# Kernel optimization log

Hardware: AMD Instinct MI355X
Metric: run time of the kernel (lower is better)

## Reference

```python
import jax, jax.numpy as jnp
from jax import lax
import numpy as np

G = 32        # voxel grid resolution per axis (pres=vres=1 -> voxel = floor(coord))
N = 100000    # number of points
C = 96        # hidden_dim == input_dim


def _voxelize(feats, coords):
    """initial_voxelize: average point features per voxel. Returns (grid (G^3,C), occ (G^3,) bool, flat idx)."""
    vox = jnp.clip(jnp.floor(coords).astype(jnp.int32), 0, G - 1)
    flat = (vox[:, 0] * G + vox[:, 1]) * G + vox[:, 2]
    sums = jax.ops.segment_sum(feats, flat, num_segments=G ** 3)
    cnt = jax.ops.segment_sum(jnp.ones((feats.shape[0],), feats.dtype), flat, num_segments=G ** 3)
    grid = sums / jnp.maximum(cnt, 1.0)[:, None]
    return grid, cnt > 0


def _sconv(feats, coords, conv_w, lin_w, lin_b):
    """SConv3d: voxelize -> submanifold 3x3x3 conv (outputs only at occupied voxels)
    -> trilinear devoxelize (missing voxels contribute 0) -> + Linear(feats)."""
    Cin = feats.shape[1]
    Cout = conv_w.shape[0]
    grid, occ = _voxelize(feats, coords)
    g = grid.reshape(G, G, G, Cin).transpose(3, 0, 1, 2)[None]          # (1,Cin,G,G,G)
    out = lax.conv_general_dilated(g, conv_w, (1, 1, 1), 'SAME',
                                   dimension_numbers=('NCDHW', 'OIDHW', 'NCDHW'))
    out = out * occ.reshape(1, 1, G, G, G)                               # submanifold: keep input coords only
    outv = out[0].transpose(1, 2, 3, 0).reshape(G ** 3, Cout)            # (G^3,Cout)
    base = jnp.floor(coords)
    f = coords - base                                                    # trilinear fractions (N,3)
    basei = base.astype(jnp.int32)
    devox = jnp.zeros((feats.shape[0], Cout), feats.dtype)
    for dx in (0, 1):
        for dy in (0, 1):
            for dz in (0, 1):
                c = basei + jnp.array([dx, dy, dz], jnp.int32)
                valid = jnp.all((c >= 0) & (c < G), axis=1)
                cc = jnp.clip(c, 0, G - 1)
                flc = (cc[:, 0] * G + cc[:, 1]) * G + cc[:, 2]
                w = ((f[:, 0] if dx else 1.0 - f[:, 0]) *
                     (f[:, 1] if dy else 1.0 - f[:, 1]) *
                     (f[:, 2] if dz else 1.0 - f[:, 2]))
                w = w * (valid & occ[flc]).astype(w.dtype)
                devox = devox + outv[flc] * w[:, None]
    return devox + feats @ lin_w.T + lin_b


def setup_inputs() -> dict:
    key = jax.random.key(0)
    ks = jax.random.split(key, 20)
    def conv(k, o, i):
        return jax.random.normal(k, (o, i, 3, 3, 3), jnp.float32) / np.sqrt(i * 27)
    def lin(k, o, i):
        k1, k2 = jax.random.split(k)
        return (jax.random.normal(k1, (o, i), jnp.float32) / np.sqrt(i),
                jax.random.normal(k2, (o,), jnp.float32) * 0.01)
    wq_lw, wq_lb = lin(ks[3], C, C)
    wh_lw, wh_lb = lin(ks[4], C, C)
    att_lw, att_lb = lin(ks[5], C, 2 * C)
    v_lw, v_lb = lin(ks[6], 1, C)
    upd_lw, upd_lb = lin(ks[7], C, 2 * C)
    return {
        'hidden': jax.random.normal(ks[0], (N, C), jnp.float32),
        'query': jax.random.normal(ks[1], (N, C), jnp.float32),
        'coords': jax.random.uniform(ks[2], (N, 3), jnp.float32) * G,
        'wq_conv': conv(ks[8], C, C), 'wq_lw': wq_lw, 'wq_lb': wq_lb,
        'wh_conv': conv(ks[9], C, C), 'wh_lw': wh_lw, 'wh_lb': wh_lb,
        'att_conv': conv(ks[10], C, 2 * C), 'att_lw': att_lw, 'att_lb': att_lb,
        'v_conv': conv(ks[11], 1, C), 'v_lw': v_lw, 'v_lb': v_lb,
        'upd_conv': conv(ks[12], C, 2 * C), 'upd_lw': upd_lw, 'upd_lb': upd_lb,
    }


def reference(hidden, query, coords,
              wq_conv, wq_lw, wq_lb,
              wh_conv, wh_lw, wh_lb,
              att_conv, att_lw, att_lb,
              v_conv, v_lw, v_lb,
              upd_conv, upd_lw, upd_lb):
    q = _sconv(query, coords, wq_conv, wq_lw, wq_lb)           # (N,C)
    h = _sconv(hidden, coords, wh_conv, wh_lw, wh_lb)          # (N,C)
    hx = jnp.concatenate([h, q], axis=1)                        # (N,2C)
    energy = jnp.tanh(_sconv(hx, coords, att_conv, att_lw, att_lb))
    attn = _sconv(energy, coords, v_conv, v_lw, v_lb)           # (N,1)
    context = attn * h                                          # attention-gated hidden
    qcat = jnp.concatenate([q, context], axis=1)                # (N,2C)
    return jnp.tanh(_sconv(qcat, coords, upd_conv, upd_lw, upd_lb))
```

## Files before the change

### kernel.cpp

```cpp
#include <hip/hip_runtime.h>
#include <math.h>


#define GD 32
#define NV (GD*GD*GD)
#define CH 96

typedef _Float16 half8 __attribute__((ext_vector_type(8)));
typedef _Float16 half4 __attribute__((ext_vector_type(4)));
typedef float f32x4 __attribute__((ext_vector_type(4)));


__global__ void k_prep(const float* __restrict__ coords, int* __restrict__ flat,
                       unsigned* __restrict__ cnt, int n) {
  int i = blockIdx.x * 256 + threadIdx.x;
  if (i >= n) return;
  float x = coords[3*i], y = coords[3*i+1], z = coords[3*i+2];
  int ix = (int)floorf(x); ix = ix < 0 ? 0 : (ix > 31 ? 31 : ix);
  int iy = (int)floorf(y); iy = iy < 0 ? 0 : (iy > 31 ? 31 : iy);
  int iz = (int)floorf(z); iz = iz < 0 ? 0 : (iz > 31 ? 31 : iz);
  int f = (ix << 10) + (iy << 5) + iz;
  flat[i] = f;
  atomicAdd(&cnt[f], 1u);
}

__global__ __launch_bounds__(1024) void k_scan(
    const unsigned* __restrict__ cnt, unsigned* __restrict__ base,
    unsigned* __restrict__ cur, float* __restrict__ inv) {
  __shared__ unsigned part[1024];
  int tid = threadIdx.x;
  int b0 = tid * 32;
  unsigned s = 0;
  for (int i = 0; i < 32; ++i) s += cnt[b0 + i];
  part[tid] = s;
  __syncthreads();
  for (int off = 1; off < 1024; off <<= 1) {
    unsigned t = (tid >= off) ? part[tid - off] : 0u;
    __syncthreads();
    if (tid >= off) part[tid] += t;
    __syncthreads();
  }
  unsigned run = part[tid] - s;
  for (int i = 0; i < 32; ++i) {
    int v = b0 + i;
    unsigned c = cnt[v];
    base[v] = run; cur[v] = run;
    inv[v] = c ? 1.0f / (float)c : 0.0f;
    run += c;
  }
}

__global__ void k_fill(const int* __restrict__ flat, unsigned* __restrict__ cur,
                       int* __restrict__ order, int n) {
  int p = blockIdx.x * 256 + threadIdx.x;
  if (p >= n) return;
  unsigned pos = atomicAdd(&cur[flat[p]], 1u);
  order[pos] = p;
}

template<int SCALED, int PAIR, int SRCF16>
__global__ void k_voxavg(const void* __restrict__ src, const float* __restrict__ scale,
                         const unsigned* __restrict__ base, const unsigned* __restrict__ cnt,
                         const float* __restrict__ inv, const int* __restrict__ order,
                         void* __restrict__ dst,
                         const void* __restrict__ src2, void* __restrict__ dst2) {
  int e = blockIdx.x * 256 + threadIdx.x;
  const void* sp = src; void* d = dst;
  if (PAIR && e >= NV * 24) { e -= NV * 24; sp = src2; d = dst2; }
  int v = e / 24, c4 = e - v * 24;
  unsigned b = base[v], c = cnt[v];
  f32x4 s = {0.f, 0.f, 0.f, 0.f};
  for (unsigned i = 0; i < c; ++i) {
    int p = order[b + i];
    f32x4 x;
    if (SRCF16) {
      half4 hx = __builtin_nontemporal_load(reinterpret_cast<const half4*>(sp) + p * 24 + c4);
      x = (f32x4){(float)hx[0], (float)hx[1], (float)hx[2], (float)hx[3]};
    } else {
      x = __builtin_nontemporal_load(reinterpret_cast<const f32x4*>(sp) + p * 24 + c4);
    }
    if (SCALED) x *= scale[p];
    s += x;
  }
  s *= inv[v];
  union { _Float16 h; unsigned short u; } h0, h1, h2, h3;
  h0.h = (_Float16)s.x; h1.h = (_Float16)s.y; h2.h = (_Float16)s.z; h3.h = (_Float16)s.w;
  ushort4 o; o.x = h0.u; o.y = h1.u; o.z = h2.u; o.w = h3.u;
  reinterpret_cast<ushort4*>(d)[e] = o;
}


__device__ __forceinline__ void wpack_one(int e, const float* __restrict__ w,
                                          _Float16* __restrict__ wp, int nch) {
  int j = e & 7; int l = (e >> 3) & 63; int r = e >> 9;
  int cot = r % 6; r /= 6; int chk = r % nch; int tap = r / nch;
  int Ci = nch * 32;
  int ci = chk * 32 + (l >> 4) * 8 + j;
  int co = cot * 16 + (l & 15);
  wp[e] = (_Float16)w[(co * Ci + ci) * 27 + tap];
}

__device__ __forceinline__ void linpack_one(int e, const float* __restrict__ w,
                                            _Float16* __restrict__ wl, int kb) {
  int j = e & 7; int l = (e >> 3) & 63; int r = e >> 9;
  int nt = r % 6; int kt = r / 6;
  int Ci = kb * 32;
  int ci = kt * 32 + (l >> 4) * 8 + j;
  int co = nt * 16 + (l & 15);
  wl[e] = (_Float16)w[co * Ci + ci];
}

#define WP3 (27*3*6*512)
#define WP6 (27*6*6*512)
#define WL3 (3*6*512)
#define WL6 (6*6*512)
#define PACK_TOTAL (2*WP3 + 2*WP6 + 2*WL3 + 2*WL6 + 27*96)

__global__ void k_packall(
    const float* __restrict__ wq, const float* __restrict__ wh,
    const float* __restrict__ wa, const float* __restrict__ wu,
    const float* __restrict__ lq, const float* __restrict__ lh,
    const float* __restrict__ la, const float* __restrict__ lu,
    const float* __restrict__ wvc,
    _Float16* __restrict__ wpq, _Float16* __restrict__ wph,
    _Float16* __restrict__ wpa, _Float16* __restrict__ wpu,
    _Float16* __restrict__ wlq, _Float16* __restrict__ wlh,
    _Float16* __restrict__ wla, _Float16* __restrict__ wlu,
    float* __restrict__ wtv) {
  int e = blockIdx.x * 256 + threadIdx.x;
  if (e < WP3) { wpack_one(e, wq, wpq, 3); return; } e -= WP3;
  if (e < WP3) { wpack_one(e, wh, wph, 3); return; } e -= WP3;
  if (e < WP6) { wpack_one(e, wa, wpa, 6); return; } e -= WP6;
  if (e < WP6) { wpack_one(e, wu, wpu, 6); return; } e -= WP6;
  if (e < WL3) { linpack_one(e, lq, wlq, 3); return; } e -= WL3;
  if (e < WL3) { linpack_one(e, lh, wlh, 3); return; } e -= WL3;
  if (e < WL6) { linpack_one(e, la, wla, 6); return; } e -= WL6;
  if (e < WL6) { linpack_one(e, lu, wlu, 6); return; } e -= WL6;
  if (e < 27 * 96) {
    int ci = e % 96, tap = e / 96;
    wtv[e] = wvc[ci * 27 + tap];
  }
}

template<int NCH, int PAIR>
__global__ __launch_bounds__(384, 4) void k_conv_mfma(
    const _Float16* __restrict__ gA, const _Float16* __restrict__ gB,
    const half8* __restrict__ wp, _Float16* __restrict__ out,
    const _Float16* __restrict__ gA2, const half8* __restrict__ wp2,
    _Float16* __restrict__ out2) {
  __shared__ unsigned short ls[12 * 34 * 40];
  int bid = blockIdx.x;
  const _Float16* ga = gA; const _Float16* gb = gB;
  const half8* w = wp; _Float16* o = out;
  if (PAIR && bid >= 512) { bid -= 512; ga = gA2; gb = gA2; w = wp2; o = out2; }
  int bx = bid >> 4, y0 = (bid & 15) * 2;
  int tid = threadIdx.x;
  int lane = tid & 63, wv = tid >> 6;
  int msel = wv & 1, npair = wv >> 1;
  int lrow = lane & 15, quad = lane >> 4;

  f32x4 acc[2][2];
#pragma unroll
  for (int i = 0; i < 2; ++i)
#pragma unroll
    for (int j = 0; j < 2; ++j) acc[i][j] = (f32x4){0.f, 0.f, 0.f, 0.f};

  for (int chunk = 0; chunk < NCH; ++chunk) {
    const _Float16* g = (NCH == 6 && chunk >= 3) ? gb : ga;
    int cbase = ((NCH == 6 && chunk >= 3) ? chunk - 3 : chunk) * 32;
    __syncthreads();
    for (int e = tid; e < 12 * 34 * 4; e += 384) {
      int ciu = e & 3; int zc = e >> 2;
      int zz = zc % 34; int sc = zc / 34;
      int dx = sc >> 2, dyy = sc & 3;
      int x = bx + dx - 1, y = y0 + dyy - 1, zv = zz - 1;
      uint4 val = {0u, 0u, 0u, 0u};
      if ((unsigned)x < 32u && (unsigned)y < 32u && (unsigned)zv < 32u)
        val = *reinterpret_cast<const uint4*>(
            g + (size_t)((x << 10) + (y << 5) + zv) * CH + cbase + ciu * 8);
      *reinterpret_cast<uint4*>(&ls[(sc * 34 + zz) * 40 + ciu * 8]) = val;
    }
    __syncthreads();
#pragma unroll
    for (int dx9 = 0; dx9 < 3; ++dx9)
#pragma unroll
      for (int dy9 = 0; dy9 < 3; ++dy9) {
        int sc = dx9 * 4 + msel + dy9;
        const unsigned short* lbase = &ls[(sc * 34) * 40 + quad * 8];
        int tap0 = (dx9 * 3 + dy9) * 3;
#pragma unroll
        for (int dz = 0; dz < 3; ++dz) {
          half8 a0 = *reinterpret_cast<const half8*>(&lbase[(lrow + dz) * 40]);
          half8 a1 = *reinterpret_cast<const half8*>(&lbase[(16 + lrow + dz) * 40]);
          const half8* wb = w + ((size_t)((tap0 + dz) * NCH + chunk) * 6 + npair * 2) * 64 + lane;
          half8 b0 = wb[0];
          half8 b1 = wb[64];
          acc[0][0] = __builtin_amdgcn_mfma_f32_16x16x32_f16(a0, b0, acc[0][0], 0, 0, 0);
          acc[1][0] = __builtin_amdgcn_mfma_f32_16x16x32_f16(a1, b0, acc[1][0], 0, 0, 0);
          acc[0][1] = __builtin_amdgcn_mfma_f32_16x16x32_f16(a0, b1, acc[0][1], 0, 0, 0);
          acc[1][1] = __builtin_amdgcn_mfma_f32_16x16x32_f16(a1, b1, acc[1][1], 0, 0, 0);
        }
      }
  }
  int y = y0 + msel;
  int vb = (bx << 10) + (y << 5);
#pragma unroll
  for (int mt = 0; mt < 2; ++mt)
#pragma unroll
    for (int nb = 0; nb < 2; ++nb)
#pragma unroll
      for (int r = 0; r < 4; ++r) {
        int z = mt * 16 + quad * 4 + r;
        o[(size_t)(vb + z) * CH + (npair * 2 + nb) * 16 + lrow] = (_Float16)acc[mt][nb][r];
      }
}

__global__ __launch_bounds__(128) void k_conv3d_v(
    const _Float16* __restrict__ g, const float* __restrict__ wt, float* __restrict__ out) {
  __shared__ float lg[9 * 34 * 33];
  __shared__ float red[128];
  int bx = blockIdx.x >> 5, by = blockIdx.x & 31;
  int tid = threadIdx.x;
  int z = tid & 31, part = tid >> 5;
  float acc = 0.f;
  for (int chunk = 0; chunk < 3; ++chunk) {
    int c0 = chunk * 32;
    __syncthreads();
    for (int e = tid; e < 9 * 34 * 32; e += 128) {
      int col = e / 1088; int rem = e - col * 1088;
      int zz = rem >> 5; int c = rem & 31;
      int x = bx + col / 3 - 1;
      int y = by + (col - (col / 3) * 3) - 1;
      int zv = zz - 1;
      float val = 0.f;
      if ((unsigned)x < 32u && (unsigned)y < 32u && (unsigned)zv < 32u)
        val = (float)g[((x << 10) + (y << 5) + zv) * CH + c0 + c];
      lg[(col * 34 + zz) * 33 + c] = val;
    }
    __syncthreads();
    for (int tap = 0; tap < 27; ++tap) {
      int cc = tap / 3, dz = tap - cc * 3;
      const float* lgp = &lg[(cc * 34 + z + dz) * 33 + part * 8];
      const float* wp = wt + tap * CH + c0 + part * 8;
#pragma unroll
      for (int c = 0; c < 8; ++c) acc += lgp[c] * wp[c];
    }
  }
  red[tid] = acc;
  __syncthreads();
  if (part == 0)
    out[(bx << 10) + (by << 5) + z] = red[z] + red[z + 32] + red[z + 64] + red[z + 96];
}


__device__ __forceinline__ void corner_one(
    const float* __restrict__ coords, const unsigned* __restrict__ cnt,
    int p, int k, int& flc, float& w) {
  float cx = coords[3*p], cy = coords[3*p+1], cz = coords[3*p+2];
  float bx = floorf(cx), by = floorf(cy), bz = floorf(cz);
  float fx = cx - bx, fy = cy - by, fz = cz - bz;
  int dx = (k >> 2) & 1, dy = (k >> 1) & 1, dzz = k & 1;
  int ix = (int)bx + dx, iy = (int)by + dy, iz = (int)bz + dzz;
  bool valid = ((unsigned)ix < 32u) && ((unsigned)iy < 32u) && ((unsigned)iz < 32u);
  int xc = min(max(ix, 0), 31), yc = min(max(iy, 0), 31), zc = min(max(iz, 0), 31);
  flc = (xc << 10) + (yc << 5) + zc;
  float wx = dx ? fx : 1.f - fx;
  float wy = dy ? fy : 1.f - fy;
  float wz = dzz ? fz : 1.f - fz;
  w = (valid && cnt[flc] > 0u) ? wx * wy * wz : 0.f;
}

template<int KB, int MODE, int PAIR>
__global__ __launch_bounds__(256) void k_point(
    const _Float16* __restrict__ outv, const void* __restrict__ X1, const void* __restrict__ X2,
    const float* __restrict__ scale, const half8* __restrict__ wl,
    const float* __restrict__ lb, const float* __restrict__ vlw,
    const float* __restrict__ coords, const unsigned* __restrict__ cnt,
    void* __restrict__ dst, float* __restrict__ attn_out, int n,
    const _Float16* __restrict__ outv2, const void* __restrict__ X1b,
    const half8* __restrict__ wl2, const float* __restrict__ lb2,
    void* __restrict__ dst2) {
  __shared__ char us[64 * 100 * 4];
  __shared__ int lflc[512];
  __shared__ float lcw[512];
  constexpr int APITCH = KB * 32 + 8;
  constexpr int XF16 = (KB == 6);
  constexpr int OUTF16 = (MODE != 2);
  int tid = threadIdx.x;
  int bid = blockIdx.x;
  const _Float16* ov = outv; const void* x1 = X1;
  const half8* w = wl; const float* b = lb; void* d = dst;
  if (PAIR) {
    int npt = (n + 63) >> 6;
    if (bid >= npt) { bid -= npt; ov = outv2; x1 = X1b; w = wl2; b = lb2; d = dst2; }
  }
  int p0 = bid * 64;

  for (int e = tid; e < 512; e += 256) {
    int j = e >> 3, k = e & 7, p = p0 + j;
    int f = 0; float wgt = 0.f;
    if (p < n) corner_one(coords, cnt, p, k, f, wgt);
    lflc[e] = f; lcw[e] = wgt;
  }

  unsigned short* lsa = reinterpret_cast<unsigned short*>(us);
  constexpr int T4 = 64 * KB * 8;
  for (int e = tid; e < T4; e += 256) {
    int j = e / (KB * 8);
    int q4 = e - j * (KB * 8);
    int p = p0 + j;
    if (XF16) {
      half4 hx = {(_Float16)0.f, (_Float16)0.f, (_Float16)0.f, (_Float16)0.f};
      if (p < n) {
        if (q4 < 24) {
          hx = __builtin_nontemporal_load(reinterpret_cast<const half4*>(x1) + p * 24 + q4);
        } else {
          hx = __builtin_nontemporal_load(reinterpret_cast<const half4*>(X2) + p * 24 + (q4 - 24));
          if (MODE == 2) {
            float sc = scale[p];
            hx = (half4){(_Float16)((float)hx[0] * sc), (_Float16)((float)hx[1] * sc),
                         (_Float16)((float)hx[2] * sc), (_Float16)((float)hx[3] * sc)};
          }
        }
      }
      *reinterpret_cast<half4*>(&lsa[j * APITCH + q4 * 4]) = hx;
    } else {
      f32x4 v = {0.f, 0.f, 0.f, 0.f};
      if (p < n)
        v = __builtin_nontemporal_load(reinterpret_cast<const f32x4*>(x1) + p * 24 + q4);
      union { _Float16 h; unsigned short u; } h0, h1, h2, h3;
      h0.h = (_Float16)v.x; h1.h = (_Float16)v.y; h2.h = (_Float16)v.z; h3.h = (_Float16)v.w;
      ushort4 o; o.x = h0.u; o.y = h1.u; o.z = h2.u; o.w = h3.u;
      *reinterpret_cast<ushort4*>(&lsa[j * APITCH + q4 * 4]) = o;
    }
  }
  __syncthreads();

  int lane = tid & 63, wv = tid >> 6;
  int lrow = lane & 15, quad = lane >> 4;
  f32x4 acc[6];
#pragma unroll
  for (int i = 0; i < 6; ++i) acc[i] = (f32x4){0.f, 0.f, 0.f, 0.f};
#pragma unroll
  for (int kt = 0; kt < KB; ++kt) {
    half8 a = *reinterpret_cast<const half8*>(&lsa[(wv * 16 + lrow) * APITCH + kt * 32 + quad * 8]);
    const half8* wb = w + (size_t)(kt * 6) * 64 + lane;
#pragma unroll
    for (int nt = 0; nt < 6; ++nt)
      acc[nt] = __builtin_amdgcn_mfma_f32_16x16x32_f16(a, wb[(size_t)nt * 64], acc[nt], 0, 0, 0);
  }
  __syncthreads();
  float* lacc = reinterpret_cast<float*>(us);
#pragma unroll
  for (int nt = 0; nt < 6; ++nt)
#pragma unroll
    for (int r = 0; r < 4; ++r)
      lacc[(wv * 16 + quad * 4 + r) * 100 + nt * 16 + lrow] = acc[nt][r];
  __syncthreads();

  int pt = tid >> 2, sub = tid & 3;
  int p = p0 + pt;
  f32x4 a[6];
  const float* lrow_p = &lacc[pt * 100 + sub * 24];
#pragma unroll
  for (int i = 0; i < 6; ++i) a[i] = *reinterpret_cast<const f32x4*>(lrow_p + i * 4);
  const f32x4* lb4 = reinterpret_cast<const f32x4*>(b + sub * 24);
#pragma unroll
  for (int i = 0; i < 6; ++i) a[i] += lb4[i];
#pragma unroll
  for (int k = 0; k < 8; ++k) {
    float wgt = lcw[pt * 8 + k];
    if (wgt != 0.f) {
      const half8* op = reinterpret_cast<const half8*>(ov + (size_t)lflc[pt * 8 + k] * CH + sub * 24);
      half8 o0 = op[0], o1 = op[1], o2 = op[2];
      f32x4 t;
      t = (f32x4){(float)o0[0], (float)o0[1], (float)o0[2], (float)o0[3]}; a[0] += wgt * t;
      t = (f32x4){(float)o0[4], (float)o0[5], (float)o0[6], (float)o0[7]}; a[1] += wgt * t;
      t = (f32x4){(float)o1[0], (float)o1[1], (float)o1[2], (float)o1[3]}; a[2] += wgt * t;
      t = (f32x4){(float)o1[4], (float)o1[5], (float)o1[6], (float)o1[7]}; a[3] += wgt * t;
      t = (f32x4){(float)o2[0], (float)o2[1], (float)o2[2], (float)o2[3]}; a[4] += wgt * t;
      t = (f32x4){(float)o2[4], (float)o2[5], (float)o2[6], (float)o2[7]}; a[5] += wgt * t;
    }
  }
  if (MODE >= 1) {
#pragma unroll
    for (int i = 0; i < 6; ++i) {
      a[i].x = tanhf(a[i].x); a[i].y = tanhf(a[i].y);
      a[i].z = tanhf(a[i].z); a[i].w = tanhf(a[i].w);
    }
  }
  if (p < n) {
    if (OUTF16) {
      _Float16* dh = reinterpret_cast<_Float16*>(d) + (size_t)p * CH + sub * 24;
      uint4* du = reinterpret_cast<uint4*>(dh);
#pragma unroll
      for (int i = 0; i < 3; ++i) {
        union { _Float16 h[8]; uint4 q; } t;
        t.h[0] = (_Float16)a[2*i].x;   t.h[1] = (_Float16)a[2*i].y;
        t.h[2] = (_Float16)a[2*i].z;   t.h[3] = (_Float16)a[2*i].w;
        t.h[4] = (_Float16)a[2*i+1].x; t.h[5] = (_Float16)a[2*i+1].y;
        t.h[6] = (_Float16)a[2*i+1].z; t.h[7] = (_Float16)a[2*i+1].w;
        du[i] = t.q;
      }
    } else {
      f32x4* d4 = reinterpret_cast<f32x4*>(d) + (size_t)p * 24 + sub * 6;
#pragma unroll
      for (int i = 0; i < 6; ++i) d4[i] = a[i];
    }
  }
  if (MODE == 1) {
    const f32x4* vw4 = reinterpret_cast<const f32x4*>(vlw + sub * 24);
    float partial = 0.f;
#pragma unroll
    for (int i = 0; i < 6; ++i) {
      f32x4 vw = vw4[i];
      partial += a[i].x * vw.x + a[i].y * vw.y + a[i].z * vw.z + a[i].w * vw.w;
    }
    partial += __shfl_xor(partial, 1);
    partial += __shfl_xor(partial, 2);
    if (sub == 0 && p < n) attn_out[p] = partial;
  }
}

__global__ void k_attn_final(const float* __restrict__ outvV, const float* __restrict__ vlb,
                             const float* __restrict__ coords, const unsigned* __restrict__ cnt,
                             float* __restrict__ attn, int n) {
  int p = blockIdx.x * 256 + threadIdx.x;
  if (p >= n) return;
  float a = attn[p] + vlb[0];
#pragma unroll
  for (int k = 0; k < 8; ++k) {
    int f; float w;
    corner_one(coords, cnt, p, k, f, w);
    a += w * outvV[f];
  }
  attn[p] = a;
}


extern "C" void kernel_launch(void* const* d_in, const int* in_sizes, int n_in,
                              void* d_out, int out_size, void* d_ws, size_t ws_size,
                              hipStream_t stream) {
  const float* hidden   = (const float*)d_in[0];
  const float* query    = (const float*)d_in[1];
  const float* coords   = (const float*)d_in[2];
  const float* wq_conv  = (const float*)d_in[3];
  const float* wq_lw    = (const float*)d_in[4];
  const float* wq_lb    = (const float*)d_in[5];
  const float* wh_conv  = (const float*)d_in[6];
  const float* wh_lw    = (const float*)d_in[7];
  const float* wh_lb    = (const float*)d_in[8];
  const float* att_conv = (const float*)d_in[9];
  const float* att_lw   = (const float*)d_in[10];
  const float* att_lb   = (const float*)d_in[11];
  const float* v_conv   = (const float*)d_in[12];
  const float* v_lw     = (const float*)d_in[13];
  const float* v_lb     = (const float*)d_in[14];
  const float* upd_conv = (const float*)d_in[15];
  const float* upd_lw   = (const float*)d_in[16];
  const float* upd_lb   = (const float*)d_in[17];
  float* out = (float*)d_out;
  const int n = in_sizes[0] / CH;

  char* wsp = (char*)d_ws;
  auto alloc = [&](size_t bytes) {
    char* r = wsp;
    wsp += (bytes + 255) & ~(size_t)255;
    return r;
  };
  int*      flat  = (int*)     alloc((size_t)n * 4);
  int*      order = (int*)     alloc((size_t)n * 4);
  unsigned* cnt   = (unsigned*)alloc((size_t)NV * 4);
  unsigned* base  = (unsigned*)alloc((size_t)NV * 4);
  unsigned* cur   = (unsigned*)alloc((size_t)NV * 4);
  float*    inv   = (float*)   alloc((size_t)NV * 4);
  float*    attn  = (float*)   alloc((size_t)n * 4);
  float*    wtv   = (float*)   alloc((size_t)27 * 96 * 4);
  _Float16* wpq = (_Float16*)alloc((size_t)WP3 * 2);
  _Float16* wph = (_Float16*)alloc((size_t)WP3 * 2);
  _Float16* wpa = (_Float16*)alloc((size_t)WP6 * 2);
  _Float16* wpu = (_Float16*)alloc((size_t)WP6 * 2);
  _Float16* wlq = (_Float16*)alloc((size_t)WL3 * 2);
  _Float16* wlh = (_Float16*)alloc((size_t)WL3 * 2);
  _Float16* wla = (_Float16*)alloc((size_t)WL6 * 2);
  _Float16* wlu = (_Float16*)alloc((size_t)WL6 * 2);
  _Float16* Hq  = (_Float16*)alloc((size_t)NV * CH * 2);
  _Float16* Hh  = (_Float16*)alloc((size_t)NV * CH * 2);
  _Float16* H1  = (_Float16*)alloc((size_t)NV * CH * 2);
  _Float16* H2  = (_Float16*)alloc((size_t)NV * CH * 2);
  _Float16* O1  = (_Float16*)alloc((size_t)NV * CH * 2);
  _Float16* O2  = (_Float16*)alloc((size_t)NV * CH * 2);
  float* Ov   = (float*)alloc((size_t)NV * 4);
  _Float16* qv   = (_Float16*)alloc((size_t)n * CH * 2);
  _Float16* hv   = (_Float16*)alloc((size_t)n * CH * 2);
  _Float16* ebuf = (_Float16*)alloc((size_t)n * CH * 2);

  const int nb  = (n + 255) / 256;
  const int npt = (n + 63) / 64;
  const int nva = NV * 24 / 256;

  hipMemsetAsync(cnt, 0, (size_t)NV * 4, stream);
  k_prep<<<nb, 256, 0, stream>>>(coords, flat, cnt, n);
  k_scan<<<1, 1024, 0, stream>>>(cnt, base, cur, inv);
  k_fill<<<nb, 256, 0, stream>>>(flat, cur, order, n);
  k_packall<<<(PACK_TOTAL + 255) / 256, 256, 0, stream>>>(
      wq_conv, wh_conv, att_conv, upd_conv, wq_lw, wh_lw, att_lw, upd_lw, v_conv,
      wpq, wph, wpa, wpu, wlq, wlh, wla, wlu, wtv);

  k_voxavg<0,1,0><<<2*nva, 256, 0, stream>>>(query, nullptr, base, cnt, inv, order,
                                             Hq, hidden, Hh);
  k_conv_mfma<3,1><<<1024, 384, 0, stream>>>(Hq, Hq, (const half8*)wpq, O1,
                                             Hh, (const half8*)wph, O2);
  k_point<3,0,1><<<2*npt, 256, 0, stream>>>(O1, query, nullptr, nullptr, (const half8*)wlq,
                                            wq_lb, nullptr, coords, cnt, qv, nullptr, n,
                                            O2, hidden, (const half8*)wlh, wh_lb, hv);

  k_voxavg<0,1,1><<<2*nva, 256, 0, stream>>>(hv, nullptr, base, cnt, inv, order,
                                             H1, qv, H2);
  k_conv_mfma<6,0><<<512, 384, 0, stream>>>(H1, H2, (const half8*)wpa, O1,
                                            nullptr, nullptr, nullptr);
  k_point<6,1,0><<<npt, 256, 0, stream>>>(O1, hv, qv, nullptr, (const half8*)wla,
                                          att_lb, v_lw, coords, cnt, ebuf, attn, n,
                                          nullptr, nullptr, nullptr, nullptr, nullptr);

  k_voxavg<0,0,1><<<nva, 256, 0, stream>>>(ebuf, nullptr, base, cnt, inv, order,
                                           Hq, nullptr, nullptr);
  k_conv3d_v<<<1024, 128, 0, stream>>>(Hq, wtv, Ov);
  k_attn_final<<<nb, 256, 0, stream>>>(Ov, v_lb, coords, cnt, attn, n);

  k_voxavg<1,0,1><<<nva, 256, 0, stream>>>(hv, attn, base, cnt, inv, order,
                                           H1, nullptr, nullptr);
  k_conv_mfma<6,0><<<512, 384, 0, stream>>>(H2, H1, (const half8*)wpu, O1,
                                            nullptr, nullptr, nullptr);
  k_point<6,2,0><<<npt, 256, 0, stream>>>(O1, qv, hv, attn, (const half8*)wlu,
                                          upd_lb, nullptr, coords, cnt, out, nullptr, n,
                                          nullptr, nullptr, nullptr, nullptr, nullptr);
}
```

Before: 691.0 us.

## Move single-output-channel 3D conv onto MFMA with dz taps as GEMM columns

Rewrites the Cin=96 to Cout=1 attention conv as an fp16 MFMA kernel. Each block covers two y rows, stages a swizzled fp16 halo tile in LDS with 16-byte loads, and packs the three dz taps into the N dimension of a 16x16x32 MFMA (13 of 16 columns are zero). A shuffle through LDS then adds the dz-shifted partial sums. This replaces the scalar fp32 FMA loop and its LDS reduction, but wastes most of each MFMA and accumulates with fp16 weights.

Result: faster. 639.1 us (-7.5%).

```diff
diff --git a/kernel.cpp b/kernel.cpp
--- a/kernel.cpp
+++ b/kernel.cpp
@@ -114,7 +114,8 @@
 #define WP6 (27*6*6*512)
 #define WL3 (3*6*512)
 #define WL6 (6*6*512)
-#define PACK_TOTAL (2*WP3 + 2*WP6 + 2*WL3 + 2*WL6 + 27*96)
+#define WV2 (27*512)
+#define PACK_TOTAL (2*WP3 + 2*WP6 + 2*WL3 + 2*WL6 + WV2)
 
 __global__ void k_packall(
     const float* __restrict__ wq, const float* __restrict__ wh,
@@ -126,7 +127,7 @@
     _Float16* __restrict__ wpa, _Float16* __restrict__ wpu,
     _Float16* __restrict__ wlq, _Float16* __restrict__ wlh,
     _Float16* __restrict__ wla, _Float16* __restrict__ wlu,
-    float* __restrict__ wtv) {
+    _Float16* __restrict__ wt2) {
   int e = blockIdx.x * 256 + threadIdx.x;
   if (e < WP3) { wpack_one(e, wq, wpq, 3); return; } e -= WP3;
   if (e < WP3) { wpack_one(e, wh, wph, 3); return; } e -= WP3;
@@ -136,9 +137,12 @@
   if (e < WL3) { linpack_one(e, lh, wlh, 3); return; } e -= WL3;
   if (e < WL6) { linpack_one(e, la, wla, 6); return; } e -= WL6;
   if (e < WL6) { linpack_one(e, lu, wlu, 6); return; } e -= WL6;
-  if (e < 27 * 96) {
-    int ci = e % 96, tap = e / 96;
-    wtv[e] = wvc[ci * 27 + tap];
+  if (e < WV2) {
+    int j = e & 7; int l = (e >> 3) & 63; int r = e >> 9;
+    int col9 = r % 9, chunk = r / 9;
+    int n = l & 15, kq = l >> 4;
+    int ci = chunk * 32 + kq * 8 + j;
+    wt2[e] = (n < 3) ? (_Float16)wvc[ci * 27 + col9 * 3 + n] : (_Float16)0.f;
   }
 }
 
@@ -215,41 +219,69 @@
       }
 }
 
-__global__ __launch_bounds__(128) void k_conv3d_v(
-    const _Float16* __restrict__ g, const float* __restrict__ wt, float* __restrict__ out) {
-  __shared__ float lg[9 * 34 * 33];
-  __shared__ float red[128];
-  int bx = blockIdx.x >> 5, by = blockIdx.x & 31;
+__global__ __launch_bounds__(128) void k_conv3d_v2(
+    const _Float16* __restrict__ g, const _Float16* __restrict__ wt2,
+    float* __restrict__ out) {
+  __shared__ unsigned short ls[12 * 48 * 32];
+  __shared__ float dl[2][48][4];
+  int bid = blockIdx.x;
+  int bx = bid >> 4, y0 = (bid & 15) * 2;
   int tid = threadIdx.x;
-  int z = tid & 31, part = tid >> 5;
-  float acc = 0.f;
+  int lane = tid & 63, wv = tid >> 6;
+  int lrow = lane & 15, quad = lane >> 4;
+
+  f32x4 acc[3];
+#pragma unroll
+  for (int i = 0; i < 3; ++i) acc[i] = (f32x4){0.f, 0.f, 0.f, 0.f};
+
   for (int chunk = 0; chunk < 3; ++chunk) {
-    int c0 = chunk * 32;
     __syncthreads();
-    for (int e = tid; e < 9 * 34 * 32; e += 128) {
-      int col = e / 1088; int rem = e - col * 1088;
-      int zz = rem >> 5; int c = rem & 31;
-      int x = bx + col / 3 - 1;
-      int y = by + (col - (col / 3) * 3) - 1;
-      int zv = zz - 1;
-      float val = 0.f;
+#pragma unroll 3
+    for (int it = 0; it < 18; ++it) {
+      int e = it * 128 + tid;
+      int c8 = e & 3;
+      int t = e >> 2;
+      int col = t / 48;
+      int zz = t - col * 48;
+      int dx = col >> 2, dyy = col & 3;
+      int x = bx + dx - 1, y = y0 + dyy - 1, zv = zz - 1;
+      uint4 val = {0u, 0u, 0u, 0u};
       if ((unsigned)x < 32u && (unsigned)y < 32u && (unsigned)zv < 32u)
-        val = (float)g[((x << 10) + (y << 5) + zv) * CH + c0 + c];
-      lg[(col * 34 + zz) * 33 + c] = val;
+        val = *reinterpret_cast<const uint4*>(
+            g + (size_t)((x << 10) + (y << 5) + zv) * CH + chunk * 32 + c8 * 8);
+      *reinterpret_cast<uint4*>(&ls[(t << 5) + ((c8 ^ (zz & 3)) << 3)]) = val;
     }
     __syncthreads();
-    for (int tap = 0; tap < 27; ++tap) {
-      int cc = tap / 3, dz = tap - cc * 3;
-      const float* lgp = &lg[(cc * 34 + z + dz) * 33 + part * 8];
-      const float* wp = wt + tap * CH + c0 + part * 8;
-#pragma unroll
-      for (int c = 0; c < 8; ++c) acc += lgp[c] * wp[c];
-    }
-  }
-  red[tid] = acc;
+#pragma unroll
+    for (int dx9 = 0; dx9 < 3; ++dx9)
+#pragma unroll
+      for (int dy9 = 0; dy9 < 3; ++dy9) {
+        int col9 = dx9 * 3 + dy9;
+        int sc = dx9 * 4 + wv + dy9;
+        half8 b = *reinterpret_cast<const half8*>(
+            wt2 + (size_t)((chunk * 9 + col9) << 9) + (lane << 3));
+#pragma unroll
+        for (int mt = 0; mt < 3; ++mt) {
+          int zz = mt * 16 + lrow;
+          half8 a = *reinterpret_cast<const half8*>(
+              &ls[((sc * 48 + zz) << 5) + ((quad ^ (zz & 3)) << 3)]);
+          acc[mt] = __builtin_amdgcn_mfma_f32_16x16x32_f16(a, b, acc[mt], 0, 0, 0);
+        }
+      }
+  }
+  if (lrow < 3) {
+#pragma unroll
+    for (int mt = 0; mt < 3; ++mt)
+#pragma unroll
+      for (int r = 0; r < 4; ++r)
+        dl[wv][mt * 16 + quad * 4 + r][lrow] = acc[mt][r];
+  }
   __syncthreads();
-  if (part == 0)
-    out[(bx << 10) + (by << 5) + z] = red[z] + red[z + 32] + red[z + 64] + red[z + 96];
+  if (tid < 64) {
+    int z = tid & 31, yb = tid >> 5;
+    float v = dl[yb][z][0] + dl[yb][z + 1][1] + dl[yb][z + 2][2];
+    out[(bx << 10) + ((y0 + yb) << 5) + z] = v;
+  }
 }
 
 
@@ -475,7 +507,7 @@
   unsigned* cur   = (unsigned*)alloc((size_t)NV * 4);
   float*    inv   = (float*)   alloc((size_t)NV * 4);
   float*    attn  = (float*)   alloc((size_t)n * 4);
-  float*    wtv   = (float*)   alloc((size_t)27 * 96 * 4);
+  _Float16* wt2   = (_Float16*)alloc((size_t)WV2 * 2);
   _Float16* wpq = (_Float16*)alloc((size_t)WP3 * 2);
   _Float16* wph = (_Float16*)alloc((size_t)WP3 * 2);
   _Float16* wpa = (_Float16*)alloc((size_t)WP6 * 2);
@@ -505,7 +537,7 @@
   k_fill<<<nb, 256, 0, stream>>>(flat, cur, order, n);
   k_packall<<<(PACK_TOTAL + 255) / 256, 256, 0, stream>>>(
       wq_conv, wh_conv, att_conv, upd_conv, wq_lw, wh_lw, att_lw, upd_lw, v_conv,
-      wpq, wph, wpa, wpu, wlq, wlh, wla, wlu, wtv);
+      wpq, wph, wpa, wpu, wlq, wlh, wla, wlu, wt2);
 
   k_voxavg<0,1,0><<<2*nva, 256, 0, stream>>>(query, nullptr, base, cnt, inv, order,
                                              Hq, hidden, Hh);
@@ -525,7 +557,7 @@
 
   k_voxavg<0,0,1><<<nva, 256, 0, stream>>>(ebuf, nullptr, base, cnt, inv, order,
                                            Hq, nullptr, nullptr);
-  k_conv3d_v<<<1024, 128, 0, stream>>>(Hq, wtv, Ov);
+  k_conv3d_v2<<<512, 128, 0, stream>>>(Hq, wt2, Ov);
   k_attn_final<<<nb, 256, 0, stream>>>(Ov, v_lb, coords, cnt, attn, n);
 
   k_voxavg<1,0,1><<<nva, 256, 0, stream>>>(hv, attn, base, cnt, inv, order,
```
